# Kernel tuning notes

Hardware: AMD Instinct MI355X
Metric: run time of the kernel (lower is better)

The kernel has to match this reference:

```python
import jax, jax.numpy as jnp
import numpy as np

NUM_HARMONICS = 64
SAMPLE_RATE = 48000
TWO_PI = 2.0 * np.pi


def setup_inputs() -> dict:
    key = jax.random.key(0)
    k1, k2, k3 = jax.random.split(key, 3)
    B, N, H = 8, 96000, NUM_HARMONICS
    # f0 in a realistic vocal/instrument range ~ [80, 480] Hz
    f0_hz = 80.0 + 400.0 * jax.random.uniform(k1, (B, N), dtype=jnp.float32)
    amp_harm = jax.random.uniform(k2, (B, N, H), dtype=jnp.float32)
    phase = jax.random.normal(k3, (B, H), dtype=jnp.float32)
    return {"f0_hz": f0_hz, "amp_harm": amp_harm, "phase": phase}


def reference(f0_hz, amp_harm, phase):
    # f0_hz: (B, N); amp_harm: (B, N, H); phase: (B, H)
    H = amp_harm.shape[-1]
    omega = (TWO_PI / SAMPLE_RATE) * f0_hz                      # (B, N)
    harm_idx = jnp.arange(1, H + 1, dtype=f0_hz.dtype)          # (H,)
    omega_h = omega[..., None] * harm_idx                       # (B, N, H)
    phases = jnp.cumsum(omega_h, axis=1) + phase[:, None, :]    # (B, N, H)
    y = jnp.einsum('bnh,bnh->bn', amp_harm, jnp.sin(phases))    # (B, N)
    phase_out = jnp.remainder(phases[:, -1, :], TWO_PI)         # (B, H)
    return (y, phase_out)
```

## Files before the change

kernel.cpp:

```cpp
#include <hip/hip_runtime.h>
#include <cstdint>
#include <cstddef>


#define B   8
#define N   96000
#define H   64
#define CH  768
#define NCH 125
#define G   3

static_assert(CH * NCH == N, "chunking");
static_assert(G * 256 == CH, "scan layout");

static constexpr double TWO_PI_D     = 6.2831853071795864769252867665590057684;
static constexpr double INV_TWO_PI_D = 1.0 / TWO_PI_D;
static constexpr double OMEGA_D      = TWO_PI_D / 48000.0;

__device__ __forceinline__ float wrap2pi_f(double v) {
  double r = v - TWO_PI_D * floor(v * INV_TWO_PI_D);
  return (float)r;
}

__global__ __launch_bounds__(256) void k_chunk_sums(const float* __restrict__ f0,
                                                    double* __restrict__ csum) {
  const int blk = blockIdx.x;
  const int b = blk / NCH, c = blk - b * NCH;
  const float* p = f0 + (size_t)b * N + (size_t)c * CH;
  const int tid = threadIdx.x;

  double s = 0.0;
#pragma unroll
  for (int j = 0; j < G; ++j) s += OMEGA_D * (double)p[tid + j * 256];

  for (int off = 32; off > 0; off >>= 1) s += __shfl_down(s, off);

  __shared__ double sw[4];
  const int lane = tid & 63, wv = tid >> 6;
  if (lane == 0) sw[wv] = s;
  __syncthreads();
  if (tid == 0) csum[blk] = sw[0] + sw[1] + sw[2] + sw[3];
}

__global__ void k_scan(double* __restrict__ csum) {
  const int b = threadIdx.x;
  if (b < B) {
    double a = 0.0;
    double* p = csum + (size_t)b * NCH;
    for (int c = 0; c < NCH; ++c) { double t = p[c]; p[c] = a; a += t; }
  }
}

__global__ __launch_bounds__(256) void k_main(const float* __restrict__ f0,
                                              const float* __restrict__ amp,
                                              const float* __restrict__ phase,
                                              const double* __restrict__ cpre,
                                              float* __restrict__ out) {
  const int blk = blockIdx.x;
  const int b = blk / NCH, c = blk - b * NCH;
  const int tid = threadIdx.x;
  const int lane = tid & 63, wv = tid >> 6;
  const size_t base = (size_t)b * N + (size_t)c * CH;

  __shared__ float  s_w[CH];
  __shared__ double s_warp[4];
  __shared__ double s_last;

  const float* f0p = f0 + base;
  const double l0 = OMEGA_D * (double)f0p[tid * G + 0];
  const double l1 = OMEGA_D * (double)f0p[tid * G + 1];
  const double l2 = OMEGA_D * (double)f0p[tid * G + 2];
  const double ts = l0 + l1 + l2;

  double x = ts;
#pragma unroll
  for (int off = 1; off < 64; off <<= 1) {
    double y = __shfl_up(x, off);
    if (lane >= off) x += y;
  }
  if (lane == 63) s_warp[wv] = x;
  __syncthreads();
  if (tid == 0) {
    double a = 0.0;
#pragma unroll
    for (int w = 0; w < 4; ++w) { double t = s_warp[w]; s_warp[w] = a; a += t; }
  }
  __syncthreads();

  double run = cpre[blk] + s_warp[wv] + (x - ts);
  const double o0 = run + l0;
  const double o1 = o0 + l1;
  const double o2 = o1 + l2;
  s_w[tid * G + 0] = wrap2pi_f(o0);
  s_w[tid * G + 1] = wrap2pi_f(o1);
  s_w[tid * G + 2] = wrap2pi_f(o2);
  if (tid == 255) s_last = o2;
  __syncthreads();

  const int hq = lane & 15;
  const int sl = lane >> 4;
  const float m0 = (float)(hq * 4 + 1), m1 = (float)(hq * 4 + 2);
  const float m2 = (float)(hq * 4 + 3), m3 = (float)(hq * 4 + 4);
  const float* phb = phase + b * H;
  const float p0 = phb[hq * 4 + 0], p1 = phb[hq * 4 + 1];
  const float p2 = phb[hq * 4 + 2], p3 = phb[hq * 4 + 3];

  const float4* ampb = reinterpret_cast<const float4*>(amp) + base * (H / 4);
  float* yb = out + base;

  for (int i0 = 0; i0 < CH; i0 += 16) {
    const int nl = i0 + (wv << 2) + sl;
    const float w = s_w[nl];
    const float4 a4 = ampb[(size_t)nl * (H / 4) + hq];

    float acc;
    acc  = a4.x * __sinf(fmaf(w, m0, p0));
    acc += a4.y * __sinf(fmaf(w, m1, p1));
    acc += a4.z * __sinf(fmaf(w, m2, p2));
    acc += a4.w * __sinf(fmaf(w, m3, p3));

    acc += __shfl_xor(acc, 1);
    acc += __shfl_xor(acc, 2);
    acc += __shfl_xor(acc, 4);
    acc += __shfl_xor(acc, 8);
    if (hq == 0) yb[nl] = acc;
  }

  if (c == NCH - 1 && tid < H) {
    const double arg = s_last * (double)(tid + 1) + (double)phase[b * H + tid];
    double r = arg - TWO_PI_D * floor(arg * INV_TWO_PI_D);
    if (r < 0.0) r += TWO_PI_D;
    if (r >= TWO_PI_D) r -= TWO_PI_D;
    out[(size_t)B * N + b * H + tid] = (float)r;
  }
}

extern "C" void kernel_launch(void* const* d_in, const int* in_sizes, int n_in,
                              void* d_out, int out_size, void* d_ws, size_t ws_size,
                              hipStream_t stream) {
  const float* f0    = (const float*)d_in[0];
  const float* amp   = (const float*)d_in[1];
  const float* phase = (const float*)d_in[2];
  float* out = (float*)d_out;
  double* csum = (double*)d_ws;

  k_chunk_sums<<<B * NCH, 256, 0, stream>>>(f0, csum);
  k_scan<<<1, 64, 0, stream>>>(csum);
  k_main<<<B * NCH, 256, 0, stream>>>(f0, amp, phase, csum, out);
}
```

Baseline: 46.67 us.

## Drop scan kernel, compute chunk prefix in main kernel, prefetch amplitudes early

Removes the single-block serial scan launch. Each main-kernel block now sums the preceding chunk totals itself with a wavefront reduction over at most 128 entries. It also issues the first eight amplitude float4 loads before the phase scan and its barriers, so memory latency overlaps the scan work. The remaining loop is unrolled by four. This saves one launch and a serial dependency in exchange for redundant per-block reads of csum and higher register pressure from the prefetch buffer.

```diff
diff --git a/kernel.cpp b/kernel.cpp
--- a/kernel.cpp
+++ b/kernel.cpp
@@ -9,9 +9,11 @@
 #define CH  768
 #define NCH 125
 #define G   3
+#define PF  8
 
 static_assert(CH * NCH == N, "chunking");
 static_assert(G * 256 == CH, "scan layout");
+static_assert(NCH <= 128, "predecessor sum uses 2 loads/lane");
 
 static constexpr double TWO_PI_D     = 6.2831853071795864769252867665590057684;
 static constexpr double INV_TWO_PI_D = 1.0 / TWO_PI_D;
@@ -42,19 +44,10 @@
   if (tid == 0) csum[blk] = sw[0] + sw[1] + sw[2] + sw[3];
 }
 
-__global__ void k_scan(double* __restrict__ csum) {
-  const int b = threadIdx.x;
-  if (b < B) {
-    double a = 0.0;
-    double* p = csum + (size_t)b * NCH;
-    for (int c = 0; c < NCH; ++c) { double t = p[c]; p[c] = a; a += t; }
-  }
-}
-
 __global__ __launch_bounds__(256) void k_main(const float* __restrict__ f0,
                                               const float* __restrict__ amp,
                                               const float* __restrict__ phase,
-                                              const double* __restrict__ cpre,
+                                              const double* __restrict__ csum,
                                               float* __restrict__ out) {
   const int blk = blockIdx.x;
   const int b = blk / NCH, c = blk - b * NCH;
@@ -64,12 +57,35 @@
 
   __shared__ float  s_w[CH];
   __shared__ double s_warp[4];
+  __shared__ double s_pre;
   __shared__ double s_last;
 
   const float* f0p = f0 + base;
-  const double l0 = OMEGA_D * (double)f0p[tid * G + 0];
-  const double l1 = OMEGA_D * (double)f0p[tid * G + 1];
-  const double l2 = OMEGA_D * (double)f0p[tid * G + 2];
+  const float f0v0 = f0p[tid * G + 0];
+  const float f0v1 = f0p[tid * G + 1];
+  const float f0v2 = f0p[tid * G + 2];
+
+  const int hq = lane & 15;
+  const int sl = lane >> 4;
+  const float4* ampb = reinterpret_cast<const float4*>(amp) + base * (H / 4);
+  float4 pf[PF];
+#pragma unroll
+  for (int j = 0; j < PF; ++j) {
+    const int nl = j * 16 + (wv << 2) + sl;
+    pf[j] = ampb[(size_t)nl * (H / 4) + hq];
+  }
+
+  if (wv == 0) {
+    double pre = 0.0;
+    if (lane < c)      pre  = csum[b * NCH + lane];
+    if (lane + 64 < c) pre += csum[b * NCH + lane + 64];
+    for (int off = 32; off > 0; off >>= 1) pre += __shfl_xor(pre, off);
+    if (lane == 0) s_pre = pre;
+  }
+
+  const double l0 = OMEGA_D * (double)f0v0;
+  const double l1 = OMEGA_D * (double)f0v1;
+  const double l2 = OMEGA_D * (double)f0v2;
   const double ts = l0 + l1 + l2;
 
   double x = ts;
@@ -87,7 +103,7 @@
   }
   __syncthreads();
 
-  double run = cpre[blk] + s_warp[wv] + (x - ts);
+  const double run = s_pre + s_warp[wv] + (x - ts);
   const double o0 = run + l0;
   const double o1 = o0 + l1;
   const double o2 = o1 + l2;
@@ -97,28 +113,40 @@
   if (tid == 255) s_last = o2;
   __syncthreads();
 
-  const int hq = lane & 15;
-  const int sl = lane >> 4;
   const float m0 = (float)(hq * 4 + 1), m1 = (float)(hq * 4 + 2);
   const float m2 = (float)(hq * 4 + 3), m3 = (float)(hq * 4 + 4);
   const float* phb = phase + b * H;
   const float p0 = phb[hq * 4 + 0], p1 = phb[hq * 4 + 1];
   const float p2 = phb[hq * 4 + 2], p3 = phb[hq * 4 + 3];
-
-  const float4* ampb = reinterpret_cast<const float4*>(amp) + base * (H / 4);
   float* yb = out + base;
 
-  for (int i0 = 0; i0 < CH; i0 += 16) {
-    const int nl = i0 + (wv << 2) + sl;
+#pragma unroll
+  for (int j = 0; j < PF; ++j) {
+    const int nl = j * 16 + (wv << 2) + sl;
     const float w = s_w[nl];
-    const float4 a4 = ampb[(size_t)nl * (H / 4) + hq];
-
+    const float4 a4 = pf[j];
     float acc;
     acc  = a4.x * __sinf(fmaf(w, m0, p0));
     acc += a4.y * __sinf(fmaf(w, m1, p1));
     acc += a4.z * __sinf(fmaf(w, m2, p2));
     acc += a4.w * __sinf(fmaf(w, m3, p3));
+    acc += __shfl_xor(acc, 1);
+    acc += __shfl_xor(acc, 2);
+    acc += __shfl_xor(acc, 4);
+    acc += __shfl_xor(acc, 8);
+    if (hq == 0) yb[nl] = acc;
+  }
 
+#pragma unroll 4
+  for (int i0 = PF * 16; i0 < CH; i0 += 16) {
+    const int nl = i0 + (wv << 2) + sl;
+    const float w = s_w[nl];
+    const float4 a4 = ampb[(size_t)nl * (H / 4) + hq];
+    float acc;
+    acc  = a4.x * __sinf(fmaf(w, m0, p0));
+    acc += a4.y * __sinf(fmaf(w, m1, p1));
+    acc += a4.z * __sinf(fmaf(w, m2, p2));
+    acc += a4.w * __sinf(fmaf(w, m3, p3));
     acc += __shfl_xor(acc, 1);
     acc += __shfl_xor(acc, 2);
     acc += __shfl_xor(acc, 4);
@@ -145,6 +173,5 @@
   double* csum = (double*)d_ws;
 
   k_chunk_sums<<<B * NCH, 256, 0, stream>>>(f0, csum);
-  k_scan<<<1, 64, 0, stream>>>(csum);
   k_main<<<B * NCH, 256, 0, stream>>>(f0, amp, phase, csum, out);
 }
```

Result: faster. 40.32 us (-13.6%).
